# Performance work log

Measured on AMD Instinct MI355X. Metric: run time of the kernel, lower is better.

## Reference

```python
import jax, jax.numpy as jnp
import numpy as np

N_HOPS = 3
EDGE_RATE = 0.5   # quirk: floor(rate+u)==1 KEEPS an edge with prob=rate, scaled by 1/(1-rate)
MESS_RATE = 0.1   # standard dropout: zero with prob p, scale kept by 1/(1-p)
N_USERS = 50000
N_ITEMS = 100000
N_NODES = N_USERS + N_ITEMS
NNZ = 1000000
D = 64


def setup_inputs() -> dict:
    key = jax.random.key(0)
    k_u, k_i, k_r, k_c, k_v = jax.random.split(key, 5)
    return {
        "user_embed": jax.random.normal(k_u, (N_USERS, D), dtype=jnp.float32),
        "item_embed": jax.random.normal(k_i, (N_ITEMS, D), dtype=jnp.float32),
        "rows": jax.random.randint(k_r, (NNZ,), 0, N_NODES),
        "cols": jax.random.randint(k_c, (NNZ,), 0, N_NODES),
        "vals": jax.random.uniform(k_v, (NNZ,), dtype=jnp.float32),
    }


def reference(user_embed, item_embed, rows, cols, vals):
    n_users = user_embed.shape[0]
    n_nodes = n_users + item_embed.shape[0]

    all_embed = jnp.concatenate([user_embed, item_embed], axis=0)  # [N, D]
    agg = all_embed
    embs = [all_embed]

    key = jax.random.key(42)
    for hop in range(N_HOPS):
        key, k_e, k_m = jax.random.split(key, 3)
        # edge dropout (faithful to torch._sparse_dropout): keep iff floor(rate+u)==1
        u = jax.random.uniform(k_e, (vals.shape[0],), dtype=vals.dtype)
        keep = (EDGE_RATE + u) >= 1.0
        v = jnp.where(keep, vals, jnp.zeros_like(vals)) * (1.0 / (1.0 - EDGE_RATE))
        # SpMM: out[r] += v * agg[c]  (zeroed edges contribute nothing, same math as
        # rebuilding a smaller sparse tensor, without dynamic shapes)
        msgs = v[:, None] * agg[cols]                       # [nnz, D]
        agg = jax.ops.segment_sum(msgs, rows, num_segments=n_nodes)
        # message dropout (nn.Dropout): zero with prob p, scale kept by 1/(1-p)
        m = jax.random.bernoulli(k_m, 1.0 - MESS_RATE, agg.shape)
        agg = jnp.where(m, agg / (1.0 - MESS_RATE), jnp.zeros_like(agg))
        embs.append(agg)

    embs = jnp.stack(embs, axis=1)  # [N, n_hops+1, D]
    return embs[:n_users], embs[n_users:]
```

## Files before the change

### kernel.cpp

```cpp
#include <hip/hip_runtime.h>
#include <stdint.h>


static constexpr int kUsers = 50000;
static constexpr int kItems = 100000;
static constexpr int kNodes = kUsers + kItems;
static constexpr int kNnz   = 1000000;
static constexpr int kD     = 64;
static constexpr int kHops  = 3;
static constexpr int kRowF  = (kHops + 1) * kD;

static constexpr int kScanBlocks = 147;
static constexpr int kCntN       = kScanBlocks * 1024;

static constexpr int kEPB     = 8192;
static constexpr int kChunks  = (kNnz + kEPB - 1) / kEPB;
static constexpr int kRowsPerGrp = kNodes / 8;

__host__ __device__ inline void tf2x32(uint32_t k0, uint32_t k1,
                                       uint32_t x0, uint32_t x1,
                                       uint32_t &o0, uint32_t &o1) {
  uint32_t ks2 = k0 ^ k1 ^ 0x1BD11BDAu;
  x0 += k0; x1 += k1;
#define TF_R(r) { x0 += x1; x1 = (x1 << (r)) | (x1 >> (32 - (r))); x1 ^= x0; }
  TF_R(13) TF_R(15) TF_R(26) TF_R(6)   x0 += k1;  x1 += ks2 + 1u;
  TF_R(17) TF_R(29) TF_R(16) TF_R(24)  x0 += ks2; x1 += k0 + 2u;
  TF_R(13) TF_R(15) TF_R(26) TF_R(6)   x0 += k0;  x1 += k1 + 3u;
  TF_R(17) TF_R(29) TF_R(16) TF_R(24)  x0 += k1;  x1 += ks2 + 4u;
  TF_R(13) TF_R(15) TF_R(26) TF_R(6)   x0 += ks2; x1 += k0 + 5u;
#undef TF_R
  o0 = x0; o1 = x1;
}

__device__ inline uint32_t jax_bits32(uint32_t k0, uint32_t k1, uint32_t i) {
  uint32_t b1, b2;
  tf2x32(k0, k1, 0u, i, b1, b2);
  return b1 ^ b2;
}

__device__ inline float bits_to_unit(uint32_t b) {
  return __uint_as_float((b >> 9) | 0x3f800000u) - 1.0f;
}


__global__ __launch_bounds__(256) void init_slice0(
    const float4* __restrict__ user, const float4* __restrict__ item,
    float4* __restrict__ out, int4* __restrict__ cnt4) {
  int i = blockIdx.x * 256 + threadIdx.x;
  if (i < kCntN / 4) cnt4[i] = make_int4(0, 0, 0, 0);
  if (i >= kNodes * 16) return;
  int node = i >> 4, q = i & 15;
  float4 v = (node < kUsers) ? user[node * 16 + q]
                             : item[(node - kUsers) * 16 + q];
  out[(size_t)node * (kRowF / 4) + q] = v;
}

__global__ __launch_bounds__(256) void hist_rec(
    const int* __restrict__ rows, const int* __restrict__ cols,
    const float* __restrict__ vals, int* __restrict__ cnt,
    uint2* __restrict__ rec,
    uint32_t e00, uint32_t e01, uint32_t e10, uint32_t e11,
    uint32_t e20, uint32_t e21) {
  int e = blockIdx.x * 256 + threadIdx.x;
  if (e >= kNnz) return;
  atomicAdd(&cnt[rows[e]], 1);
  float u0 = bits_to_unit(jax_bits32(e00, e01, (uint32_t)e));
  float u1 = bits_to_unit(jax_bits32(e10, e11, (uint32_t)e));
  float u2 = bits_to_unit(jax_bits32(e20, e21, (uint32_t)e));
  uint32_t packed = (uint32_t)cols[e]
                  | ((0.5f + u0 >= 1.0f) ? (1u << 29) : 0u)
                  | ((0.5f + u1 >= 1.0f) ? (1u << 30) : 0u)
                  | ((0.5f + u2 >= 1.0f) ? (1u << 31) : 0u);
  rec[e] = make_uint2(packed, __float_as_uint(vals[e] * 2.0f));
}

__global__ __launch_bounds__(256) void scanA(
    const int* __restrict__ cnt, int* __restrict__ partials) {
  int t = threadIdx.x;
  int4 v = ((const int4*)(cnt + blockIdx.x * 1024))[t];
  int s = v.x + v.y + v.z + v.w;
  __shared__ int sh[256];
  sh[t] = s; __syncthreads();
  for (int off = 128; off > 0; off >>= 1) {
    if (t < off) sh[t] += sh[t + off];
    __syncthreads();
  }
  if (t == 0) partials[blockIdx.x] = sh[0];
}

__global__ __launch_bounds__(256) void scanB(int* __restrict__ partials) {
  int t = threadIdx.x;
  int v = (t < kScanBlocks) ? partials[t] : 0;
  __shared__ int sh[256];
  sh[t] = v; __syncthreads();
  for (int off = 1; off < 256; off <<= 1) {
    int a = (t >= off) ? sh[t - off] : 0;
    __syncthreads();
    sh[t] += a;
    __syncthreads();
  }
  if (t < kScanBlocks) partials[t] = sh[t] - v;
}

__global__ __launch_bounds__(256) void scanC(
    int* __restrict__ cnt, const int* __restrict__ partials) {
  int t = threadIdx.x;
  int4 v = ((const int4*)(cnt + blockIdx.x * 1024))[t];
  int s = v.x + v.y + v.z + v.w;
  __shared__ int sh[256];
  sh[t] = s; __syncthreads();
  for (int off = 1; off < 256; off <<= 1) {
    int a = (t >= off) ? sh[t - off] : 0;
    __syncthreads();
    sh[t] += a;
    __syncthreads();
  }
  int base = partials[blockIdx.x] + sh[t] - s;
  int4 o;
  o.x = base; o.y = base + v.x; o.z = o.y + v.y; o.w = o.z + v.z;
  ((int4*)(cnt + blockIdx.x * 1024))[t] = o;
}

__global__ __launch_bounds__(256) void route_scatter(
    const int* __restrict__ rows, const uint2* __restrict__ rec,
    int* __restrict__ X, uint2* __restrict__ ed) {
  const int grp   = blockIdx.x & 7;
  const int chunk = blockIdx.x >> 3;
  const int lo = grp * kRowsPerGrp;
  const int hi = lo + kRowsPerGrp;
  const int base4 = chunk * (kEPB / 4);
  const int t = threadIdx.x;
#pragma unroll
  for (int k = 0; k < kEPB / 4 / 256; ++k) {
    int idx4 = base4 + k * 256 + t;
    if (idx4 >= kNnz / 4) break;
    int4 r4 = ((const int4*)rows)[idx4];
    int e0 = idx4 * 4;
    int rr[4] = {r4.x, r4.y, r4.z, r4.w};
#pragma unroll
    for (int j = 0; j < 4; ++j) {
      int r = rr[j];
      if (r >= lo && r < hi) {
        int pos = atomicAdd(&X[r], 1);
        ed[pos] = rec[e0 + j];
      }
    }
  }
}

__global__ __launch_bounds__(256) void csr_spmm(
    const int* __restrict__ X, const uint2* __restrict__ ed,
    float* __restrict__ out, int hop, uint32_t km0, uint32_t km1) {
  int pair = blockIdx.x * 4 + (threadIdx.x >> 6);
  int rA = pair * 2;
  if (rA >= kNodes) return;
  int lane = threadIdx.x & 63;
  int g = lane >> 3, q = lane & 7;
  int sA = (rA == 0) ? 0 : X[rA - 1];
  int tA = X[rA];
  int tB = X[rA + 1];
  float uA = bits_to_unit(jax_bits32(km0, km1, (uint32_t)(rA * kD + lane)));
  float uB = bits_to_unit(jax_bits32(km0, km1, (uint32_t)((rA + 1) * kD + lane)));
  float mA = (uA < 0.9f) ? (1.0f / 0.9f) : 0.0f;
  float mB = (uB < 0.9f) ? (1.0f / 0.9f) : 0.0f;
  float4 a0 = make_float4(0.f, 0.f, 0.f, 0.f);
  float4 a1 = make_float4(0.f, 0.f, 0.f, 0.f);
  float4 b0 = make_float4(0.f, 0.f, 0.f, 0.f);
  float4 b1 = make_float4(0.f, 0.f, 0.f, 0.f);
  const float* src = out + (size_t)hop * kD;
  const uint32_t kbit = 1u << (29 + hop);
  int iA = sA + g, iB = tA + g;
  while (iA < tA || iB < tB) {
    if (iA < tA) {
      uint2 m = ed[iA];
      if (m.x & kbit) {
        float v = __uint_as_float(m.y);
        const float* p = src + (size_t)(m.x & 0x3FFFFu) * kRowF + (q << 3);
        float4 x0 = *(const float4*)p;
        float4 x1 = *(const float4*)(p + 4);
        a0.x += v * x0.x; a0.y += v * x0.y; a0.z += v * x0.z; a0.w += v * x0.w;
        a1.x += v * x1.x; a1.y += v * x1.y; a1.z += v * x1.z; a1.w += v * x1.w;
      }
      iA += 8;
    }
    if (iB < tB) {
      uint2 m = ed[iB];
      if (m.x & kbit) {
        float v = __uint_as_float(m.y);
        const float* p = src + (size_t)(m.x & 0x3FFFFu) * kRowF + (q << 3);
        float4 x0 = *(const float4*)p;
        float4 x1 = *(const float4*)(p + 4);
        b0.x += v * x0.x; b0.y += v * x0.y; b0.z += v * x0.z; b0.w += v * x0.w;
        b1.x += v * x1.x; b1.y += v * x1.y; b1.z += v * x1.z; b1.w += v * x1.w;
      }
      iB += 8;
    }
  }
#pragma unroll
  for (int msk = 8; msk <= 32; msk <<= 1) {
    a0.x += __shfl_xor(a0.x, msk); a0.y += __shfl_xor(a0.y, msk);
    a0.z += __shfl_xor(a0.z, msk); a0.w += __shfl_xor(a0.w, msk);
    a1.x += __shfl_xor(a1.x, msk); a1.y += __shfl_xor(a1.y, msk);
    a1.z += __shfl_xor(a1.z, msk); a1.w += __shfl_xor(a1.w, msk);
    b0.x += __shfl_xor(b0.x, msk); b0.y += __shfl_xor(b0.y, msk);
    b0.z += __shfl_xor(b0.z, msk); b0.w += __shfl_xor(b0.w, msk);
    b1.x += __shfl_xor(b1.x, msk); b1.y += __shfl_xor(b1.y, msk);
    b1.z += __shfl_xor(b1.z, msk); b1.w += __shfl_xor(b1.w, msk);
  }
  float w[8];
#pragma unroll
  for (int j = 0; j < 8; ++j) {
    float wA = __shfl(mA, (q << 3) + j);
    float wB = __shfl(mB, (q << 3) + j);
    w[j] = (g == 0) ? wA : wB;
  }
  if (g < 2) {
    int r = rA + g;
    float4 r0, r1;
    if (g == 0) {
      r0 = make_float4(a0.x * w[0], a0.y * w[1], a0.z * w[2], a0.w * w[3]);
      r1 = make_float4(a1.x * w[4], a1.y * w[5], a1.z * w[6], a1.w * w[7]);
    } else {
      r0 = make_float4(b0.x * w[0], b0.y * w[1], b0.z * w[2], b0.w * w[3]);
      r1 = make_float4(b1.x * w[4], b1.y * w[5], b1.z * w[6], b1.w * w[7]);
    }
    float* dst = out + (size_t)r * kRowF + (hop + 1) * kD + (q << 3);
    *(float4*)dst = r0;
    *(float4*)(dst + 4) = r1;
  }
}

__global__ __launch_bounds__(256) void init_full(
    const float4* __restrict__ user, const float4* __restrict__ item,
    float4* __restrict__ out) {
  int i = blockIdx.x * 256 + threadIdx.x;
  if (i >= kNodes * 16) return;
  int node = i >> 4, q = i & 15;
  float4 v = (node < kUsers) ? user[node * 16 + q]
                             : item[(node - kUsers) * 16 + q];
  float4 z = make_float4(0.f, 0.f, 0.f, 0.f);
  float4* row = out + (size_t)node * (kRowF / 4);
  row[q] = v; row[16 + q] = z; row[32 + q] = z; row[48 + q] = z;
}

__global__ __launch_bounds__(256) void spmm_atomic(
    const int* __restrict__ rows, const int* __restrict__ cols,
    const float* __restrict__ vals, float* __restrict__ out, int hop,
    uint32_t k0, uint32_t k1) {
  int e = (int)((blockIdx.x * 256u + threadIdx.x) >> 6);
  if (e >= kNnz) return;
  int lane = threadIdx.x & 63;
  float u = bits_to_unit(jax_bits32(k0, k1, (uint32_t)e));
  if (!(0.5f + u >= 1.0f)) return;
  float v = vals[e] * 2.0f;
  int r = rows[e], c = cols[e];
  float msg = v * out[(size_t)c * kRowF + hop * kD + lane];
  atomicAdd(&out[(size_t)r * kRowF + (hop + 1) * kD + lane], msg);
}

__global__ __launch_bounds__(256) void mdrop_kernel(
    float* __restrict__ out, int hop, uint32_t k0, uint32_t k1) {
  const int total = kNodes * kD;
  int j = blockIdx.x * 256 + threadIdx.x;
  if (j >= total) return;
  float u = bits_to_unit(jax_bits32(k0, k1, (uint32_t)j));
  int node = j >> 6, d = j & 63;
  size_t idx = (size_t)node * kRowF + (hop + 1) * kD + d;
  float a = out[idx];
  out[idx] = (u < 0.9f) ? a / 0.9f : 0.0f;
}

extern "C" void kernel_launch(void* const* d_in, const int* in_sizes, int n_in,
                              void* d_out, int out_size, void* d_ws, size_t ws_size,
                              hipStream_t stream) {
  const float* user = (const float*)d_in[0];
  const float* item = (const float*)d_in[1];
  const int*   rows = (const int*)d_in[2];
  const int*   cols = (const int*)d_in[3];
  const float* vals = (const float*)d_in[4];
  float* out = (float*)d_out;

  uint32_t k0 = 0u, k1 = 42u;
  uint32_t ke[kHops][2], km[kHops][2];
  for (int hop = 0; hop < kHops; ++hop) {
    uint32_t n0, n1;
    tf2x32(k0, k1, 0u, 0u, n0, n1);
    tf2x32(k0, k1, 0u, 1u, ke[hop][0], ke[hop][1]);
    tf2x32(k0, k1, 0u, 2u, km[hop][0], km[hop][1]);
    k0 = n0; k1 = n1;
  }

  const size_t x_b   = (size_t)kCntN * 4;
  const size_t rec_b = ((size_t)kNnz * 8 + 4095) & ~(size_t)4095;
  const size_t ed_b  = rec_b;
  const size_t par_b = 4096;
  const size_t need  = x_b + rec_b + ed_b + par_b;

  if (ws_size >= need) {
    char* ws = (char*)d_ws;
    int*   X        = (int*)ws;
    uint2* rec      = (uint2*)(ws + x_b);
    uint2* ed       = (uint2*)(ws + x_b + rec_b);
    int*   partials = (int*)(ws + x_b + rec_b + ed_b);

    init_slice0<<<(kNodes * 16 + 255) / 256, 256, 0, stream>>>(
        (const float4*)user, (const float4*)item, (float4*)out, (int4*)X);
    hist_rec<<<(kNnz + 255) / 256, 256, 0, stream>>>(
        rows, cols, vals, X, rec,
        ke[0][0], ke[0][1], ke[1][0], ke[1][1], ke[2][0], ke[2][1]);
    scanA<<<kScanBlocks, 256, 0, stream>>>(X, partials);
    scanB<<<1, 256, 0, stream>>>(partials);
    scanC<<<kScanBlocks, 256, 0, stream>>>(X, partials);
    route_scatter<<<kChunks * 8, 256, 0, stream>>>(rows, rec, X, ed);

    const int nPairs = kNodes / 2;
    for (int hop = 0; hop < kHops; ++hop) {
      csr_spmm<<<(nPairs + 3) / 4, 256, 0, stream>>>(
          X, ed, out, hop, km[hop][0], km[hop][1]);
    }
  } else {
    init_full<<<(kNodes * 16 + 255) / 256, 256, 0, stream>>>(
        (const float4*)user, (const float4*)item, (float4*)out);
    for (int hop = 0; hop < kHops; ++hop) {
      spmm_atomic<<<(kNnz * 64 + 255) / 256, 256, 0, stream>>>(
          rows, cols, vals, out, hop, ke[hop][0], ke[hop][1]);
      mdrop_kernel<<<(kNodes * kD + 255) / 256, 256, 0, stream>>>(
          out, hop, km[hop][0], km[hop][1]);
    }
  }
}
```

Measured before the change: 270.7 us.

## Build per-hop CSR of kept edges so SpMM skips dropped edges

Instead of one CSR holding all edges with per-hop keep bits that the SpMM tests on every read, the histogram and scatter now count and route only kept edges into three separate per-hop CSR segments. The scan is extended to cover three count arrays, and the SpMM reads only the edges that survive for its hop, roughly halving edge traffic and branch divergence per hop. In exchange the scatter performs up to three atomics and writes per edge, the edge buffer grows to a fixed cap of 1.6M entries, and edges beyond that cap would be silently dropped.

```diff
diff --git a/kernel.cpp b/kernel.cpp
--- a/kernel.cpp
+++ b/kernel.cpp
@@ -10,8 +10,10 @@
 static constexpr int kHops  = 3;
 static constexpr int kRowF  = (kHops + 1) * kD;
 
-static constexpr int kScanBlocks = 147;
-static constexpr int kCntN       = kScanBlocks * 1024;
+static constexpr int kCntN        = 147 * 1024;
+static constexpr int kScanBlocks3 = 3 * 147;
+static constexpr int kCntTotal    = kScanBlocks3 * 1024;
+static constexpr int kEdCap       = 1600000;
 
 static constexpr int kEPB     = 8192;
 static constexpr int kChunks  = (kNnz + kEPB - 1) / kEPB;
@@ -47,7 +49,7 @@
     const float4* __restrict__ user, const float4* __restrict__ item,
     float4* __restrict__ out, int4* __restrict__ cnt4) {
   int i = blockIdx.x * 256 + threadIdx.x;
-  if (i < kCntN / 4) cnt4[i] = make_int4(0, 0, 0, 0);
+  if (i < kCntTotal / 4) cnt4[i] = make_int4(0, 0, 0, 0);
   if (i >= kNodes * 16) return;
   int node = i >> 4, q = i & 15;
   float4 v = (node < kUsers) ? user[node * 16 + q]
@@ -63,14 +65,20 @@
     uint32_t e20, uint32_t e21) {
   int e = blockIdx.x * 256 + threadIdx.x;
   if (e >= kNnz) return;
-  atomicAdd(&cnt[rows[e]], 1);
+  int r = rows[e];
   float u0 = bits_to_unit(jax_bits32(e00, e01, (uint32_t)e));
   float u1 = bits_to_unit(jax_bits32(e10, e11, (uint32_t)e));
   float u2 = bits_to_unit(jax_bits32(e20, e21, (uint32_t)e));
+  bool kp0 = (0.5f + u0 >= 1.0f);
+  bool kp1 = (0.5f + u1 >= 1.0f);
+  bool kp2 = (0.5f + u2 >= 1.0f);
+  if (kp0) atomicAdd(&cnt[r], 1);
+  if (kp1) atomicAdd(&cnt[kCntN + r], 1);
+  if (kp2) atomicAdd(&cnt[2 * kCntN + r], 1);
   uint32_t packed = (uint32_t)cols[e]
-                  | ((0.5f + u0 >= 1.0f) ? (1u << 29) : 0u)
-                  | ((0.5f + u1 >= 1.0f) ? (1u << 30) : 0u)
-                  | ((0.5f + u2 >= 1.0f) ? (1u << 31) : 0u);
+                  | (kp0 ? (1u << 29) : 0u)
+                  | (kp1 ? (1u << 30) : 0u)
+                  | (kp2 ? (1u << 31) : 0u);
   rec[e] = make_uint2(packed, __float_as_uint(vals[e] * 2.0f));
 }
 
@@ -88,18 +96,18 @@
   if (t == 0) partials[blockIdx.x] = sh[0];
 }
 
-__global__ __launch_bounds__(256) void scanB(int* __restrict__ partials) {
+__global__ __launch_bounds__(512) void scanB(int* __restrict__ partials) {
   int t = threadIdx.x;
-  int v = (t < kScanBlocks) ? partials[t] : 0;
-  __shared__ int sh[256];
+  int v = (t < kScanBlocks3) ? partials[t] : 0;
+  __shared__ int sh[512];
   sh[t] = v; __syncthreads();
-  for (int off = 1; off < 256; off <<= 1) {
+  for (int off = 1; off < 512; off <<= 1) {
     int a = (t >= off) ? sh[t - off] : 0;
     __syncthreads();
     sh[t] += a;
     __syncthreads();
   }
-  if (t < kScanBlocks) partials[t] = sh[t] - v;
+  if (t < kScanBlocks3) partials[t] = sh[t] - v;
 }
 
 __global__ __launch_bounds__(256) void scanC(
@@ -141,8 +149,19 @@
     for (int j = 0; j < 4; ++j) {
       int r = rr[j];
       if (r >= lo && r < hi) {
-        int pos = atomicAdd(&X[r], 1);
-        ed[pos] = rec[e0 + j];
+        uint2 m = rec[e0 + j];
+        if (m.x & (1u << 29)) {
+          int pos = atomicAdd(&X[r], 1);
+          if (pos < kEdCap) ed[pos] = m;
+        }
+        if (m.x & (1u << 30)) {
+          int pos = atomicAdd(&X[kCntN + r], 1);
+          if (pos < kEdCap) ed[pos] = m;
+        }
+        if (m.x & (1u << 31)) {
+          int pos = atomicAdd(&X[2 * kCntN + r], 1);
+          if (pos < kEdCap) ed[pos] = m;
+        }
       }
     }
   }
@@ -156,9 +175,10 @@
   if (rA >= kNodes) return;
   int lane = threadIdx.x & 63;
   int g = lane >> 3, q = lane & 7;
-  int sA = (rA == 0) ? 0 : X[rA - 1];
-  int tA = X[rA];
-  int tB = X[rA + 1];
+  int idx0 = hop * kCntN + rA;
+  int sA = (idx0 == 0) ? 0 : X[idx0 - 1];
+  int tA = X[idx0];
+  int tB = X[idx0 + 1];
   float uA = bits_to_unit(jax_bits32(km0, km1, (uint32_t)(rA * kD + lane)));
   float uB = bits_to_unit(jax_bits32(km0, km1, (uint32_t)((rA + 1) * kD + lane)));
   float mA = (uA < 0.9f) ? (1.0f / 0.9f) : 0.0f;
@@ -168,31 +188,26 @@
   float4 b0 = make_float4(0.f, 0.f, 0.f, 0.f);
   float4 b1 = make_float4(0.f, 0.f, 0.f, 0.f);
   const float* src = out + (size_t)hop * kD;
-  const uint32_t kbit = 1u << (29 + hop);
   int iA = sA + g, iB = tA + g;
   while (iA < tA || iB < tB) {
     if (iA < tA) {
       uint2 m = ed[iA];
-      if (m.x & kbit) {
-        float v = __uint_as_float(m.y);
-        const float* p = src + (size_t)(m.x & 0x3FFFFu) * kRowF + (q << 3);
-        float4 x0 = *(const float4*)p;
-        float4 x1 = *(const float4*)(p + 4);
-        a0.x += v * x0.x; a0.y += v * x0.y; a0.z += v * x0.z; a0.w += v * x0.w;
-        a1.x += v * x1.x; a1.y += v * x1.y; a1.z += v * x1.z; a1.w += v * x1.w;
-      }
+      float v = __uint_as_float(m.y);
+      const float* p = src + (size_t)(m.x & 0x3FFFFu) * kRowF + (q << 3);
+      float4 x0 = *(const float4*)p;
+      float4 x1 = *(const float4*)(p + 4);
+      a0.x += v * x0.x; a0.y += v * x0.y; a0.z += v * x0.z; a0.w += v * x0.w;
+      a1.x += v * x1.x; a1.y += v * x1.y; a1.z += v * x1.z; a1.w += v * x1.w;
       iA += 8;
     }
     if (iB < tB) {
       uint2 m = ed[iB];
-      if (m.x & kbit) {
-        float v = __uint_as_float(m.y);
-        const float* p = src + (size_t)(m.x & 0x3FFFFu) * kRowF + (q << 3);
-        float4 x0 = *(const float4*)p;
-        float4 x1 = *(const float4*)(p + 4);
-        b0.x += v * x0.x; b0.y += v * x0.y; b0.z += v * x0.z; b0.w += v * x0.w;
-        b1.x += v * x1.x; b1.y += v * x1.y; b1.z += v * x1.z; b1.w += v * x1.w;
-      }
+      float v = __uint_as_float(m.y);
+      const float* p = src + (size_t)(m.x & 0x3FFFFu) * kRowF + (q << 3);
+      float4 x0 = *(const float4*)p;
+      float4 x1 = *(const float4*)(p + 4);
+      b0.x += v * x0.x; b0.y += v * x0.y; b0.z += v * x0.z; b0.w += v * x0.w;
+      b1.x += v * x1.x; b1.y += v * x1.y; b1.z += v * x1.z; b1.w += v * x1.w;
       iB += 8;
     }
   }
@@ -290,9 +305,9 @@
     k0 = n0; k1 = n1;
   }
 
-  const size_t x_b   = (size_t)kCntN * 4;
+  const size_t x_b   = (size_t)kCntTotal * 4;
   const size_t rec_b = ((size_t)kNnz * 8 + 4095) & ~(size_t)4095;
-  const size_t ed_b  = rec_b;
+  const size_t ed_b  = (size_t)kEdCap * 8;
   const size_t par_b = 4096;
   const size_t need  = x_b + rec_b + ed_b + par_b;
 
@@ -308,9 +323,9 @@
     hist_rec<<<(kNnz + 255) / 256, 256, 0, stream>>>(
         rows, cols, vals, X, rec,
         ke[0][0], ke[0][1], ke[1][0], ke[1][1], ke[2][0], ke[2][1]);
-    scanA<<<kScanBlocks, 256, 0, stream>>>(X, partials);
-    scanB<<<1, 256, 0, stream>>>(partials);
-    scanC<<<kScanBlocks, 256, 0, stream>>>(X, partials);
+    scanA<<<kScanBlocks3, 256, 0, stream>>>(X, partials);
+    scanB<<<1, 512, 0, stream>>>(partials);
+    scanC<<<kScanBlocks3, 256, 0, stream>>>(X, partials);
     route_scatter<<<kChunks * 8, 256, 0, stream>>>(rows, rec, X, ed);
 
     const int nPairs = kNodes / 2;
```

Result: slower. 312.7 us (+15.5%).
